# Performance work log

Hardware: AMD Instinct MI355X
Metric: run time of the kernel (lower is better)

## Reference

```python
import jax, jax.numpy as jnp
from jax import lax
import numpy as np

N = 128      # number of dictionary atoms (ConvTranspose in_channels)
K = 16       # kernel size
S = 8        # stride
R_LR = 0.1   # SGD lr on codes R
LMDA = 0.005 # soft-threshold level
MAX_ITER = 20  # cap on ISTA iterations (torch loop is uncapped)


def conv_t(R, W):
    """torch ConvTranspose2d(N,1,K,stride=S,bias=False) with weight W[N,1,K,K].
    Implemented as a fractionally-strided conv: transpose to OIHW and flip spatial."""
    Wt = jnp.flip(jnp.transpose(W, (1, 0, 2, 3)), axis=(2, 3))  # [1,N,K,K]
    return lax.conv_general_dilated(
        R, Wt,
        window_strides=(1, 1),
        padding=[(K - 1, K - 1), (K - 1, K - 1)],
        lhs_dilation=(S, S),
        dimension_numbers=("NCHW", "OIHW", "NCHW"),
    )  # [B,1,D,D] with D=(c-1)*S+K


def ista(img, W):
    B, D = img.shape[0], img.shape[2]
    c = (D - K) // S + 1
    R0 = jnp.zeros((B, N, c, c), img.dtype)

    loss_grad = jax.grad(lambda r: jnp.sum((img - conv_t(r, W)) ** 2))

    def cond(state):
        _, i, converged = state
        return jnp.logical_and(jnp.logical_not(converged), i < MAX_ITER)

    def body(state):
        R, i, _ = state
        g = loss_grad(R)                       # dL/dR
        Rn = R - R_LR * g                      # SGD step
        Rn = jax.nn.relu(Rn - LMDA) - jax.nn.relu(-Rn - LMDA)  # soft threshold
        converged = jnp.linalg.norm(Rn - R) / jnp.linalg.norm(R) < 0.01
        return (Rn, i + 1, converged)

    R, _, _ = lax.while_loop(cond, body, (R0, jnp.int32(0), jnp.bool_(False)))
    return R


def setup_inputs() -> dict:
    key = jax.random.key(0)
    k1, k2 = jax.random.split(key)
    img = jax.random.normal(k1, (128, 1, 128, 128), jnp.float32)
    W = jax.random.normal(k2, (N, 1, K, K), jnp.float32)
    # normalize_weights(): unit L2 norm per atom (flatten over out_ch,K,K)
    W = W / jnp.linalg.norm(W.reshape(N, -1), axis=1).reshape(N, 1, 1, 1)
    return {"img_batch": img, "U_weight": W}


def reference(img_batch, U_weight):
    R = ista(img_batch, U_weight)
    return conv_t(R, U_weight)
```

## Files before the change

### kernel.cpp

```cpp
#include <hip/hip_runtime.h>
#include <stdint.h>

#define BATCH 128
#define NAT   128
#define DIM   128
#define CP    17
#define MAXIT 20
#define STEP  0.2f
#define LMD   0.005f
#define NGRAD 900

typedef short bf16x8 __attribute__((ext_vector_type(8)));
typedef float f32x16 __attribute__((ext_vector_type(16)));

#define SZ_RP (BATCH*CP*CP*NAT)
#define SZ_RS (BATCH*DIM*DIM)
#define O_RP   0
#define O_RSH  (O_RP + SZ_RP*2)
#define O_W2H  (O_RSH + SZ_RS*2)
#define O_W2L  (O_W2H + 64*512*2)
#define O_WTH  (O_W2L + 64*512*2)
#define O_WTL  (O_WTH + 128*256*2)
#define O_PART (O_WTL + 128*256*2)
#define O_IMB  (O_PART + 4096*4)

#define GLOAD16(gp, lp) __builtin_amdgcn_global_load_lds( \
    (const __attribute__((address_space(1))) uint32_t*)(gp), \
    (__attribute__((address_space(3))) uint32_t*)(lp), 16, 0, 0)

__device__ __forceinline__ void split2(float x, ushort& h, ushort& l) {
    uint32_t u = __float_as_uint(x);
    uint32_t hr = (u + 0x7FFFu + ((u >> 16) & 1u)) >> 16;
    h = (ushort)hr;
    float r = x - __uint_as_float(hr << 16);
    uint32_t u2 = __float_as_uint(r);
    l = (ushort)((u2 + 0x7FFFu + ((u2 >> 16) & 1u)) >> 16);
}
__device__ __forceinline__ float us2f(ushort u) {
    return __uint_as_float(((uint32_t)u) << 16);
}
__device__ __forceinline__ uint pk(ushort a, ushort b) {
    return (uint)a | ((uint)b << 16);
}
__device__ __forceinline__ ushort f2bf(float x) {
    uint32_t u = __float_as_uint(x);
    return (ushort)((u + 0x7FFFu + ((u >> 16) & 1u)) >> 16);
}

__global__ void kzero(uint4* __restrict__ rp) {
    int i = blockIdx.x * 256 + threadIdx.x;
    rp[i] = uint4{0u, 0u, 0u, 0u};
}

__global__ void kprep(const float* __restrict__ W,
                      ushort* __restrict__ wth, ushort* __restrict__ wtl,
                      ushort* __restrict__ w2h, ushort* __restrict__ w2l) {
    int tid = blockIdx.x * 256 + threadIdx.x;
    int n = tid >> 8, kk = tid & 255;
    ushort h, l; split2(W[tid], h, l);
    wth[tid] = h; wtl[tid] = l;
    int kx = kk >> 4, ky = kk & 15;
    int uv = (kx & 7) * 8 + (ky & 7);
    int k2 = ((kx >> 3) * 2 + (ky >> 3)) * 128 + n;
    w2h[uv * 512 + k2] = h; w2l[uv * 512 + k2] = l;
}

__global__ void kinit0(const float* __restrict__ img, ushort* __restrict__ rsh,
                       ushort* __restrict__ imb) {
    int t8 = (blockIdx.x * 256 + threadIdx.x) * 8;
    uint hw[4];
#pragma unroll
    for (int v = 0; v < 2; ++v) {
        float4 im = *(const float4*)&img[t8 + v * 4];
        hw[v*2+0] = pk(f2bf(im.x), f2bf(im.y));
        hw[v*2+1] = pk(f2bf(im.z), f2bf(im.w));
    }
    uint4 pkd{hw[0], hw[1], hw[2], hw[3]};
    *(uint4*)&rsh[t8] = pkd;
    *(uint4*)&imb[t8] = pkd;
}

__global__ __launch_bounds__(256) void kconvt(
    const ushort* __restrict__ rp, const ushort* __restrict__ w2h,
    const ushort* __restrict__ imb, ushort* __restrict__ rsh)
{
    const int tid = threadIdx.x;
    __shared__ uint4 lds[4096];
    const int bx = blockIdx.x;
    const int bid = ((bx & 7) << 6) | (bx >> 3);
    const int m0 = bid * 64;
    const int lane = tid & 63, w = tid >> 6;
    const int wm = w >> 1, wn = w & 1, g = lane >> 5;
    const int u = (lane & 7) ^ ((lane >> 3) & 7);

    const int b0 = m0 >> 8;
    const int x0 = ((m0 & 255) >> 4) * 8;
    const int erow = tid >> 3, ec0 = (tid & 7) * 16;
    const int ebase = b0 * DIM * DIM + (x0 + erow) * DIM + ec0;
    uint4 ib0 = *(const uint4*)&imb[ebase];
    uint4 ib1 = *(const uint4*)&imb[ebase + 8];
    __builtin_amdgcn_sched_barrier(0);

    int off0[4]; const ushort* srcp[4];
#pragma unroll
    for (int i = 0; i < 4; ++i) {
        int s = w * 4 + i;
        if (s < 8) {
            int ml = s * 8 + (lane >> 3);
            int mm = m0 + ml;
            int b_ = mm >> 8, cell = mm & 255, px0 = cell >> 4, py0 = cell & 15;
            off0[i] = ((b_ * CP + px0 + 1) * CP + py0 + 1) * NAT + u * 8;
            srcp[i] = rp;
        } else {
            int ml = (s - 8) * 8 + (lane >> 3);
            off0[i] = ml * 512 + u * 8;
            srcp[i] = w2h;
        }
    }
    auto stage = [&](int kc, int buf) {
        int ij = kc >> 1;
        int dA = (kc & 1) * 64 - ((ij >> 1) * CP + (ij & 1)) * NAT;
        int dB = kc * 64;
        uint4* base = lds + buf * 1024;
#pragma unroll
        for (int i = 0; i < 4; ++i) {
            int s = w * 4 + i;
            GLOAD16(srcp[i] + off0[i] + (s < 8 ? dA : dB), base + s * 64);
        }
    };

    f32x16 acc = {};
    const int arow = wm * 32 + (lane & 31);
    const int brow = wn * 32 + (lane & 31);
    const int ax = lane & 7;

    stage(0, 0); stage(1, 1); stage(2, 2);
    for (int kc = 0; kc < 8; ++kc) {
        if (kc < 5) stage(kc + 3, (kc + 3) & 3);
        int nf = 7 - kc; nf = nf > 3 ? 3 : nf;
        switch (nf) {
            case 3: asm volatile("s_waitcnt vmcnt(12)" ::: "memory"); break;
            case 2: asm volatile("s_waitcnt vmcnt(8)"  ::: "memory"); break;
            case 1: asm volatile("s_waitcnt vmcnt(4)"  ::: "memory"); break;
            default: asm volatile("s_waitcnt vmcnt(0)" ::: "memory"); break;
        }
        __builtin_amdgcn_s_barrier();
        __builtin_amdgcn_sched_barrier(0);
        const uint4* Lb = lds + (kc & 3) * 1024;
#pragma unroll
        for (int ks = 0; ks < 4; ++ks) {
            int un = (ks * 2 + g) ^ ax;
            bf16x8 Ah = __builtin_bit_cast(bf16x8, Lb[      arow * 8 + un]);
            bf16x8 Bh = __builtin_bit_cast(bf16x8, Lb[512 + brow * 8 + un]);
            acc = __builtin_amdgcn_mfma_f32_32x32x16_bf16(Ah, Bh, acc, 0, 0, 0);
        }
        __builtin_amdgcn_sched_barrier(0);
        __builtin_amdgcn_s_barrier();
    }

    float* ldsO = (float*)lds;
    const int uvx = wn * 32 + (lane & 31);
    const int uu = uvx >> 3, vv = uvx & 7;
#pragma unroll
    for (int r = 0; r < 16; ++r) {
        int mr = m0 + wm * 32 + (r & 3) + 8 * (r >> 2) + 4 * g;
        int cl = mr & 255;
        ldsO[(((cl >> 4) & 3) * 8 + uu) * 129 + (cl & 15) * 8 + vv] = acc[r];
    }
    __syncthreads();
    const float* lrow = &ldsO[erow * 129 + ec0];
    const uint* iw0 = (const uint*)&ib0;
    const uint* iw1 = (const uint*)&ib1;
    uint hw[8];
#pragma unroll
    for (int w4 = 0; w4 < 4; ++w4) {
        hw[w4] = pk(f2bf(us2f((ushort)iw0[w4])         - lrow[2 * w4 + 0]),
                    f2bf(us2f((ushort)(iw0[w4] >> 16)) - lrow[2 * w4 + 1]));
        hw[4 + w4] = pk(f2bf(us2f((ushort)iw1[w4])         - lrow[8 + 2 * w4 + 0]),
                        f2bf(us2f((ushort)(iw1[w4] >> 16)) - lrow[8 + 2 * w4 + 1]));
    }
    *(uint4*)&rsh[ebase]     = uint4{hw[0],hw[1],hw[2],hw[3]};
    *(uint4*)&rsh[ebase + 8] = uint4{hw[4],hw[5],hw[6],hw[7]};
}

__global__ __launch_bounds__(256) void kgrad(
    const ushort* __restrict__ rsh, const ushort* __restrict__ wth,
    ushort* __restrict__ rp, float* __restrict__ partials, int t)
{
    __shared__ uint4 lds[2048];
    __shared__ float red0[16];
    __shared__ int sg;
    const int tid = threadIdx.x;
    const int bx = blockIdx.x;
    const int xcd = bx & 7;
    const int bid = (xcd < 2 ? xcd * 57 : 114 + (xcd - 2) * 56) + (bx >> 3);
    const int m0 = bid * 64;
    const int n0 = blockIdx.y * 64;
    const int lane = tid & 63, w = tid >> 6;
    const int wm = w >> 1, wn = w & 1, g = lane >> 5;
    const int u = (lane & 7) ^ ((lane >> 3) & 7);
    const int pb2 = blockIdx.y * 450 + bid;
    const float* bankO = partials + ((t - 1) & 1) * 2048;
    float* bankN = partials + (t & 1) * 2048;

    float gd[4] = {0.f, 0.f, 0.f, 0.f}, gr[4] = {0.f, 0.f, 0.f, 0.f};
    float pod = 0.f, por = 0.f;
    if (t >= 1) {
#pragma unroll
        for (int k = 0; k < 4; ++k) {
            int i = tid + k * 256;
            if (i < NGRAD) { gd[k] = bankO[i]; gr[k] = bankO[1024 + i]; }
        }
        pod = bankO[pb2]; por = bankO[1024 + pb2];
    }
    int rbase0, rbase1; uint4 rv0, rv1;
    {
        int item = tid;
        int rowL = item >> 3, ch = item & 7;
        int mr = m0 + rowL;
        int bb = mr / 225, rm = mr % 225, pxx = rm / 15, pyy = rm % 15;
        rbase0 = ((bb * CP + pxx + 1) * CP + pyy + 1) * NAT + n0 + ch * 8;
        rv0 = *(const uint4*)&rp[rbase0];
    }
    {
        int item = 256 + tid;
        int rowL = item >> 3, ch = item & 7;
        int mr = m0 + rowL;
        int bb = mr / 225, rm = mr % 225, pxx = rm / 15, pyy = rm % 15;
        rbase1 = ((bb * CP + pxx + 1) * CP + pyy + 1) * NAT + n0 + ch * 8;
        rv1 = *(const uint4*)&rp[rbase1];
    }
    __builtin_amdgcn_sched_barrier(0);

    int off0[4]; const ushort* srcp[4];
#pragma unroll
    for (int i = 0; i < 4; ++i) {
        int s = w * 4 + i;
        if (s < 8) {
            int ml = s * 8 + (lane >> 3);
            int mA = m0 + ml, bA = mA / 225, rm = mA % 225, px = rm / 15, py = rm % 15;
            off0[i] = bA * DIM * DIM + (8 * px + (u >> 1)) * DIM + 8 * py + (u & 1) * 8;
            srcp[i] = rsh;
        } else {
            int ml = (s - 8) * 8 + (lane >> 3);
            off0[i] = (n0 + ml) * 256 + u * 8;
            srcp[i] = wth;
        }
    }
    auto stage = [&](int kc, int buf) {
        uint4* base = lds + buf * 1024;
#pragma unroll
        for (int i = 0; i < 4; ++i) {
            int s = w * 4 + i;
            GLOAD16(srcp[i] + off0[i] + (s < 8 ? kc * 512 : kc * 64), base + s * 64);
        }
    };

    f32x16 acc = {};
    const int arow = wm * 32 + (lane & 31);
    const int brow = wn * 32 + (lane & 31);
    const int ax = lane & 7;

    stage(0, 0);
    for (int kc = 0; kc < 4; ++kc) {
        asm volatile("s_waitcnt vmcnt(0)" ::: "memory");
        __builtin_amdgcn_s_barrier();
        __builtin_amdgcn_sched_barrier(0);
        if (kc < 3) stage(kc + 1, (kc + 1) & 1);
        const uint4* Lb = lds + (kc & 1) * 1024;
#pragma unroll
        for (int ks = 0; ks < 4; ++ks) {
            int un = (ks * 2 + g) ^ ax;
            bf16x8 Ah = __builtin_bit_cast(bf16x8, Lb[      arow * 8 + un]);
            bf16x8 Bh = __builtin_bit_cast(bf16x8, Lb[512 + brow * 8 + un]);
            acc = __builtin_amdgcn_mfma_f32_32x32x16_bf16(Ah, Bh, acc, 0, 0, 0);
        }
        __builtin_amdgcn_sched_barrier(0);
    }
    __syncthreads();

    int gate = 0;
    if (t >= 1) {
        float d2 = 0.f, r2 = 0.f;
        d2 += gd[0]; d2 += gd[1]; d2 += gd[2]; d2 += gd[3];
        r2 += gr[0]; r2 += gr[1]; r2 += gr[2]; r2 += gr[3];
        for (int off = 32; off; off >>= 1) { d2 += __shfl_down(d2, off, 64); r2 += __shfl_down(r2, off, 64); }
        int w_ = tid >> 6, l = tid & 63;
        if (l == 0) { red0[w_] = d2; red0[8 + w_] = r2; }
        __syncthreads();
        if (tid == 0) {
            float td = red0[0] + red0[1] + red0[2] + red0[3];
            float tr = red0[8] + red0[9] + red0[10] + red0[11];
            sg = (td < 1e-4f * tr) ? 1 : 0;
        }
        __syncthreads();
        gate = sg;
    }
    const bool dow = (t == 0) || (gate == 0);

    float* ldsO = (float*)lds;
    {
        const int colL = wn * 32 + (lane & 31);
#pragma unroll
        for (int r = 0; r < 16; ++r) {
            int rowL = wm * 32 + (r & 3) + 8 * (r >> 2) + 4 * g;
            ldsO[rowL * 76 + colL] = acc[r];
        }
    }
    __syncthreads();

    float d2 = 0.f, r2 = 0.f;
    if (dow) {
#pragma unroll
        for (int i = 0; i < 2; ++i) {
            int item = i * 256 + tid;
            int rowL = item >> 3, ch = item & 7;
            uint4 hv = i ? rv1 : rv0;
            int base = i ? rbase1 : rbase0;
            const float* lp = &ldsO[rowL * 76 + ch * 8];
            uint ho[4];
#pragma unroll
            for (int wd = 0; wd < 4; ++wd) {
                uint hw_ = ((const uint*)&hv)[wd];
                ushort nh0, nh1;
                {
                    float rold = us2f((ushort)hw_);
                    float v = fmaf(STEP, lp[wd * 2 + 0], rold);
                    float st = fmaxf(v - LMD, 0.f) - fmaxf(-v - LMD, 0.f);
                    nh0 = f2bf(st);
                    float df = us2f(nh0) - rold;
                    d2 += df * df; r2 += rold * rold;
                }
                {
                    float rold = us2f((ushort)(hw_ >> 16));
                    float v = fmaf(STEP, lp[wd * 2 + 1], rold);
                    float st = fmaxf(v - LMD, 0.f) - fmaxf(-v - LMD, 0.f);
                    nh1 = f2bf(st);
                    float df = us2f(nh1) - rold;
                    d2 += df * df; r2 += rold * rold;
                }
                ho[wd] = pk(nh0, nh1);
            }
            *(uint4*)&rp[base] = uint4{ho[0], ho[1], ho[2], ho[3]};
        }
    }

    for (int off = 32; off; off >>= 1) { d2 += __shfl_down(d2, off, 64); r2 += __shfl_down(r2, off, 64); }
    int w_ = tid >> 6, l = tid & 63;
    if (l == 0) { red0[w_] = d2; red0[8 + w_] = r2; }
    __syncthreads();
    if (tid == 0) {
        if (dow) {
            float td = red0[0] + red0[1] + red0[2] + red0[3];
            float tr = red0[8] + red0[9] + red0[10] + red0[11];
            bankN[pb2] = td;
            bankN[1024 + pb2] = tr;
        } else {
            bankN[pb2] = pod;
            bankN[1024 + pb2] = por;
        }
    }
}

__global__ __launch_bounds__(256) void kfinal(
    const ushort* __restrict__ rp,
    const ushort* __restrict__ w2h, const ushort* __restrict__ w2l,
    float* __restrict__ outp)
{
    const int tid = threadIdx.x;
    __shared__ uint4 lds[3072];
    const int bx = blockIdx.x;
    const int bid = ((bx & 7) << 6) | (bx >> 3);
    const int m0 = bid * 64;
    const int lane = tid & 63, w = tid >> 6;
    const int wm = w >> 1, wn = w & 1, g = lane >> 5;
    const int u = (lane & 7) ^ ((lane >> 3) & 7);

    const ushort* const srcs[3] = {rp, w2h, w2l};
    int off0[6]; const ushort* srcp[6];
#pragma unroll
    for (int i = 0; i < 6; ++i) {
        int j = w * 6 + i, p = j >> 3, jj = j & 7;
        int ml = jj * 8 + (lane >> 3);
        srcp[i] = srcs[p];
        if (p == 0) {
            int mm = m0 + ml;
            int b_ = mm >> 8, cell = mm & 255, px0 = cell >> 4, py0 = cell & 15;
            off0[i] = ((b_ * CP + px0 + 1) * CP + py0 + 1) * NAT + u * 8;
        } else {
            off0[i] = ml * 512 + u * 8;
        }
    }
    auto stage = [&](int kc, int buf) {
        int ij = kc >> 1;
        int dA = (kc & 1) * 64 - ((ij >> 1) * CP + (ij & 1)) * NAT;
        int dB = kc * 64;
#pragma unroll
        for (int i = 0; i < 6; ++i) {
            int j = w * 6 + i;
            GLOAD16(srcp[i] + off0[i] + (j < 8 ? dA : dB), lds + buf * 1536 + j * 64);
        }
    };

    f32x16 acc = {};
    const int arow = wm * 32 + (lane & 31);
    const int brow = wn * 32 + (lane & 31);
    const int ax = lane & 7;

    stage(0, 0);
    __syncthreads();
    for (int kc = 0;; ++kc) {
        const int cur = kc & 1;
        if (kc < 7) stage(kc + 1, cur ^ 1);
        const uint4* Lb = lds + cur * 1536;
#pragma unroll
        for (int ks = 0; ks < 4; ++ks) {
            int un = (ks * 2 + g) ^ ax;
            bf16x8 Ah = __builtin_bit_cast(bf16x8, Lb[       arow * 8 + un]);
            bf16x8 Bh = __builtin_bit_cast(bf16x8, Lb[512  + brow * 8 + un]);
            bf16x8 Bl = __builtin_bit_cast(bf16x8, Lb[1024 + brow * 8 + un]);
            acc = __builtin_amdgcn_mfma_f32_32x32x16_bf16(Ah, Bh, acc, 0, 0, 0);
            acc = __builtin_amdgcn_mfma_f32_32x32x16_bf16(Ah, Bl, acc, 0, 0, 0);
        }
        if (kc == 7) break;
        __syncthreads();
    }

    __syncthreads();
    float* ldsO = (float*)lds;
    const int uvx = wn * 32 + (lane & 31);
    const int uu = uvx >> 3, vv = uvx & 7;
#pragma unroll
    for (int r = 0; r < 16; ++r) {
        int mr = m0 + wm * 32 + (r & 3) + 8 * (r >> 2) + 4 * g;
        int cl = mr & 255;
        ldsO[(((cl >> 4) & 3) * 8 + uu) * 129 + (cl & 15) * 8 + vv] = acc[r];
    }
    __syncthreads();
    const int b0 = m0 >> 8;
    const int x0 = ((m0 & 255) >> 4) * 8;
    const int row = tid >> 3, c0 = (tid & 7) * 16;
    const int base = b0 * DIM * DIM + (x0 + row) * DIM + c0;
    const float* lrow = &ldsO[row * 129 + c0];
#pragma unroll
    for (int v = 0; v < 4; ++v)
        *(float4*)&outp[base + v * 4] =
            float4{lrow[v*4], lrow[v*4+1], lrow[v*4+2], lrow[v*4+3]};
}

extern "C" void kernel_launch(void* const* d_in, const int* in_sizes, int n_in,
                              void* d_out, int out_size, void* d_ws, size_t ws_size,
                              hipStream_t stream) {
    const float* img = (const float*)d_in[0];
    const float* W   = (const float*)d_in[1];
    char* ws = (char*)d_ws;
    ushort* rp  = (ushort*)(ws + O_RP);
    ushort* rsh = (ushort*)(ws + O_RSH);
    ushort* w2h = (ushort*)(ws + O_W2H);
    ushort* w2l = (ushort*)(ws + O_W2L);
    ushort* wth = (ushort*)(ws + O_WTH);
    ushort* wtl = (ushort*)(ws + O_WTL);
    float* partials = (float*)(ws + O_PART);
    ushort* imb = (ushort*)(ws + O_IMB);
    float* outp = (float*)d_out;

    kzero<<<2312, 256, 0, stream>>>((uint4*)(ws + O_RP));
    kprep<<<128, 256, 0, stream>>>(W, wth, wtl, w2h, w2l);
    kinit0<<<1024, 256, 0, stream>>>(img, rsh, imb);
    kgrad<<<dim3(450, 2), 256, 0, stream>>>(rsh, wth, rp, partials, 0);
    for (int t = 1; t < MAXIT; ++t) {
        kconvt<<<512, 256, 0, stream>>>(rp, w2h, imb, rsh);
        kgrad<<<dim3(450, 2), 256, 0, stream>>>(rsh, wth, rp, partials, t);
    }
    kfinal<<<512, 256, 0, stream>>>(rp, w2h, w2l, outp);
}
```

Baseline: 386.3 us.

## Split kconvt into single-wave blocks with barrier-free double-buffered loads

Restructures the transposed-convolution kernel from 256-thread blocks computing 64x64 tiles into 64-thread single-wave blocks, each computing a 32x32 tile, launched as 2048 blocks. With one wave per block, the s_barrier calls are replaced by waitcnt-only synchronisation, and the pipeline moves from 4-deep to 2-deep LDS buffering. This is meant to cut barrier overhead and raise occupancy and block count. In exchange, the A operand is loaded twice, once per N-half, which adds global and L2 traffic, and the shallower pipeline hides less latency.

```diff
diff --git a/kernel.cpp b/kernel.cpp
--- a/kernel.cpp
+++ b/kernel.cpp
@@ -80,107 +80,105 @@
     *(uint4*)&imb[t8] = pkd;
 }
 
-__global__ __launch_bounds__(256) void kconvt(
+__global__ __launch_bounds__(64) void kconvt(
     const ushort* __restrict__ rp, const ushort* __restrict__ w2h,
     const ushort* __restrict__ imb, ushort* __restrict__ rsh)
 {
-    const int tid = threadIdx.x;
-    __shared__ uint4 lds[4096];
+    const int lane = threadIdx.x;
+    __shared__ uint4 lds[1024];
     const int bx = blockIdx.x;
-    const int bid = ((bx & 7) << 6) | (bx >> 3);
-    const int m0 = bid * 64;
-    const int lane = tid & 63, w = tid >> 6;
-    const int wm = w >> 1, wn = w & 1, g = lane >> 5;
+    const int bid = ((bx & 7) << 8) | (bx >> 3);
+    const int mblk = bid >> 1;
+    const int q32 = (bid & 1) * 32;
+    const int m0 = mblk * 32;
+    const int b0 = mblk >> 3;
+    const int P  = (mblk & 7) * 2;
+    const int g = lane >> 5;
     const int u = (lane & 7) ^ ((lane >> 3) & 7);
 
-    const int b0 = m0 >> 8;
-    const int x0 = ((m0 & 255) >> 4) * 8;
-    const int erow = tid >> 3, ec0 = (tid & 7) * 16;
-    const int ebase = b0 * DIM * DIM + (x0 + erow) * DIM + ec0;
-    uint4 ib0 = *(const uint4*)&imb[ebase];
-    uint4 ib1 = *(const uint4*)&imb[ebase + 8];
+    int eb[2]; uint4 ib[2];
+#pragma unroll
+    for (int j = 0; j < 2; ++j) {
+        int item = j * 64 + lane;
+        int lrow = item >> 4, colc = (item & 15) * 8;
+        int px_sel = lrow >> 2, uu = lrow & 3;
+        eb[j] = b0 * (DIM * DIM) + ((P + px_sel) * 8 + (q32 >> 3) + uu) * DIM + colc;
+        ib[j] = *(const uint4*)&imb[eb[j]];
+    }
     __builtin_amdgcn_sched_barrier(0);
 
-    int off0[4]; const ushort* srcp[4];
+    int offA[4], offB[4];
 #pragma unroll
     for (int i = 0; i < 4; ++i) {
-        int s = w * 4 + i;
-        if (s < 8) {
-            int ml = s * 8 + (lane >> 3);
-            int mm = m0 + ml;
-            int b_ = mm >> 8, cell = mm & 255, px0 = cell >> 4, py0 = cell & 15;
-            off0[i] = ((b_ * CP + px0 + 1) * CP + py0 + 1) * NAT + u * 8;
-            srcp[i] = rp;
-        } else {
-            int ml = (s - 8) * 8 + (lane >> 3);
-            off0[i] = ml * 512 + u * 8;
-            srcp[i] = w2h;
-        }
+        int ml = i * 8 + (lane >> 3);
+        int cl = (m0 & 255) + ml;
+        int px0 = cl >> 4, py0 = cl & 15;
+        offA[i] = ((b0 * CP + px0 + 1) * CP + py0 + 1) * NAT + u * 8;
+        int uvl = i * 8 + (lane >> 3);
+        offB[i] = (q32 + uvl) * 512 + u * 8;
     }
     auto stage = [&](int kc, int buf) {
         int ij = kc >> 1;
         int dA = (kc & 1) * 64 - ((ij >> 1) * CP + (ij & 1)) * NAT;
         int dB = kc * 64;
-        uint4* base = lds + buf * 1024;
-#pragma unroll
-        for (int i = 0; i < 4; ++i) {
-            int s = w * 4 + i;
-            GLOAD16(srcp[i] + off0[i] + (s < 8 ? dA : dB), base + s * 64);
-        }
+        uint4* base = lds + buf * 512;
+#pragma unroll
+        for (int i = 0; i < 4; ++i) GLOAD16(rp  + offA[i] + dA, base + i * 64);
+#pragma unroll
+        for (int i = 0; i < 4; ++i) GLOAD16(w2h + offB[i] + dB, base + 256 + i * 64);
     };
 
     f32x16 acc = {};
-    const int arow = wm * 32 + (lane & 31);
-    const int brow = wn * 32 + (lane & 31);
+    const int arow = lane & 31;
     const int ax = lane & 7;
 
-    stage(0, 0); stage(1, 1); stage(2, 2);
+    stage(0, 0); stage(1, 1);
     for (int kc = 0; kc < 8; ++kc) {
-        if (kc < 5) stage(kc + 3, (kc + 3) & 3);
-        int nf = 7 - kc; nf = nf > 3 ? 3 : nf;
-        switch (nf) {
-            case 3: asm volatile("s_waitcnt vmcnt(12)" ::: "memory"); break;
-            case 2: asm volatile("s_waitcnt vmcnt(8)"  ::: "memory"); break;
-            case 1: asm volatile("s_waitcnt vmcnt(4)"  ::: "memory"); break;
-            default: asm volatile("s_waitcnt vmcnt(0)" ::: "memory"); break;
-        }
-        __builtin_amdgcn_s_barrier();
+        if (kc < 7) asm volatile("s_waitcnt vmcnt(8)" ::: "memory");
+        else        asm volatile("s_waitcnt vmcnt(0)" ::: "memory");
         __builtin_amdgcn_sched_barrier(0);
-        const uint4* Lb = lds + (kc & 3) * 1024;
+        const uint4* Lb = lds + (kc & 1) * 512;
 #pragma unroll
         for (int ks = 0; ks < 4; ++ks) {
             int un = (ks * 2 + g) ^ ax;
             bf16x8 Ah = __builtin_bit_cast(bf16x8, Lb[      arow * 8 + un]);
-            bf16x8 Bh = __builtin_bit_cast(bf16x8, Lb[512 + brow * 8 + un]);
+            bf16x8 Bh = __builtin_bit_cast(bf16x8, Lb[256 + arow * 8 + un]);
             acc = __builtin_amdgcn_mfma_f32_32x32x16_bf16(Ah, Bh, acc, 0, 0, 0);
         }
         __builtin_amdgcn_sched_barrier(0);
-        __builtin_amdgcn_s_barrier();
-    }
-
+        if (kc < 6) {
+            asm volatile("s_waitcnt lgkmcnt(0)" ::: "memory");
+            __builtin_amdgcn_sched_barrier(0);
+            stage(kc + 2, kc & 1);
+        }
+    }
+
+    asm volatile("s_waitcnt lgkmcnt(0)" ::: "memory");
+    __builtin_amdgcn_sched_barrier(0);
     float* ldsO = (float*)lds;
-    const int uvx = wn * 32 + (lane & 31);
-    const int uu = uvx >> 3, vv = uvx & 7;
+    const int uvl = lane & 31, vv = uvl & 7, uu = uvl >> 3;
 #pragma unroll
     for (int r = 0; r < 16; ++r) {
-        int mr = m0 + wm * 32 + (r & 3) + 8 * (r >> 2) + 4 * g;
-        int cl = mr & 255;
-        ldsO[(((cl >> 4) & 3) * 8 + uu) * 129 + (cl & 15) * 8 + vv] = acc[r];
-    }
-    __syncthreads();
-    const float* lrow = &ldsO[erow * 129 + ec0];
-    const uint* iw0 = (const uint*)&ib0;
-    const uint* iw1 = (const uint*)&ib1;
-    uint hw[8];
-#pragma unroll
-    for (int w4 = 0; w4 < 4; ++w4) {
-        hw[w4] = pk(f2bf(us2f((ushort)iw0[w4])         - lrow[2 * w4 + 0]),
-                    f2bf(us2f((ushort)(iw0[w4] >> 16)) - lrow[2 * w4 + 1]));
-        hw[4 + w4] = pk(f2bf(us2f((ushort)iw1[w4])         - lrow[8 + 2 * w4 + 0]),
-                        f2bf(us2f((ushort)(iw1[w4] >> 16)) - lrow[8 + 2 * w4 + 1]));
-    }
-    *(uint4*)&rsh[ebase]     = uint4{hw[0],hw[1],hw[2],hw[3]};
-    *(uint4*)&rsh[ebase + 8] = uint4{hw[4],hw[5],hw[6],hw[7]};
+        int cl = (r & 3) + 8 * (r >> 2) + 4 * g;
+        int px_sel = cl >> 4, py0 = cl & 15;
+        ldsO[(px_sel * 4 + uu) * 132 + py0 * 8 + vv] = acc[r];
+    }
+    asm volatile("s_waitcnt lgkmcnt(0)" ::: "memory");
+    __builtin_amdgcn_sched_barrier(0);
+#pragma unroll
+    for (int j = 0; j < 2; ++j) {
+        int item = j * 64 + lane;
+        int lrow = item >> 4, colc = (item & 15) * 8;
+        const float* lp = &ldsO[lrow * 132 + colc];
+        const uint* iw = (const uint*)&ib[j];
+        uint hw[4];
+#pragma unroll
+        for (int w4 = 0; w4 < 4; ++w4) {
+            hw[w4] = pk(f2bf(us2f((ushort)iw[w4])         - lp[2 * w4 + 0]),
+                        f2bf(us2f((ushort)(iw[w4] >> 16)) - lp[2 * w4 + 1]));
+        }
+        *(uint4*)&rsh[eb[j]] = uint4{hw[0], hw[1], hw[2], hw[3]};
+    }
 }
 
 __global__ __launch_bounds__(256) void kgrad(
@@ -469,7 +467,7 @@
     kinit0<<<1024, 256, 0, stream>>>(img, rsh, imb);
     kgrad<<<dim3(450, 2), 256, 0, stream>>>(rsh, wth, rp, partials, 0);
     for (int t = 1; t < MAXIT; ++t) {
-        kconvt<<<512, 256, 0, stream>>>(rp, w2h, imb, rsh);
+        kconvt<<<2048, 64, 0, stream>>>(rp, w2h, imb, rsh);
         kgrad<<<dim3(450, 2), 256, 0, stream>>>(rsh, wth, rp, partials, t);
     }
     kfinal<<<512, 256, 0, stream>>>(rp, w2h, w2l, outp);
```

Result: no change. 388.6 us (median of 2 runs) (+0.6%).
